# Kernel tuning notes

Hardware: AMD Instinct MI355X
Metric: run time of the kernel (lower is better)

Reference implementation:

```python
import jax, jax.numpy as jnp
import numpy as np

B, SQ, SK, D, H, DFF = 4, 1024, 1024, 1024, 16, 4096
DEPTH = D // H
EPS = 1e-6


def setup_inputs() -> dict:
    key = jax.random.key(0)
    ks = jax.random.split(key, 32)
    s = 0.02
    inp = {
        "x": jax.random.normal(ks[0], (B, SQ, D), jnp.float32),
        "enc_output": jax.random.normal(ks[1], (B, SK, D), jnp.float32),
        # causal look-ahead mask: 1 where attention is disallowed
        "look_ahead_mask": (1.0 - jnp.tril(jnp.ones((SQ, SQ), jnp.float32)))[None, None],
        "padding_mask": jnp.zeros((B, 1, 1, SK), jnp.float32),
    }
    names = ["wq1", "wk1", "wv1", "wo1", "wq2", "wk2", "wv2", "wo2"]
    for i, n in enumerate(names):
        inp[n] = jax.random.normal(ks[2 + i], (D, D), jnp.float32) * s
        inp["b" + n[1:]] = jnp.zeros((D,), jnp.float32)
    inp["w_ffn1"] = jax.random.normal(ks[12], (D, DFF), jnp.float32) * s
    inp["b_ffn1"] = jnp.zeros((DFF,), jnp.float32)
    inp["w_ffn2"] = jax.random.normal(ks[13], (DFF, D), jnp.float32) * s
    inp["b_ffn2"] = jnp.zeros((D,), jnp.float32)
    for i in (1, 2, 3):
        inp[f"gamma{i}"] = jnp.ones((D,), jnp.float32)
        inp[f"beta{i}"] = jnp.zeros((D,), jnp.float32)
    return inp


def _layernorm(x, gamma, beta):
    mu = jnp.mean(x, axis=-1, keepdims=True)
    var = jnp.var(x, axis=-1, keepdims=True)
    return (x - mu) * jax.lax.rsqrt(var + EPS) * gamma + beta


def _split_heads(x):
    b, s, _ = x.shape
    return x.reshape(b, s, H, DEPTH).transpose(0, 2, 1, 3)  # (B,H,S,depth)


def _mha(v_in, k_in, q_in, mask, wq, bq, wk, bk, wv, bv, wo, bo):
    q = _split_heads(q_in @ wq + bq)
    k = _split_heads(k_in @ wk + bk)
    v = _split_heads(v_in @ wv + bv)
    logits = jnp.einsum("bhqd,bhkd->bhqk", q, k) / jnp.sqrt(jnp.float32(DEPTH))
    if mask is not None:
        logits = logits + mask * -1e9
    attn = jax.nn.softmax(logits, axis=-1)
    out = jnp.einsum("bhqk,bhkd->bhqd", attn, v)
    out = out.transpose(0, 2, 1, 3).reshape(q_in.shape[0], -1, D)
    return out @ wo + bo, attn


def reference(x, enc_output, look_ahead_mask, padding_mask,
              wq1, bq1, wk1, bk1, wv1, bv1, wo1, bo1,
              wq2, bq2, wk2, bk2, wv2, bv2, wo2, bo2,
              w_ffn1, b_ffn1, w_ffn2, b_ffn2,
              gamma1, beta1, gamma2, beta2, gamma3, beta3):
    attn1, aw1 = _mha(x, x, x, look_ahead_mask,
                      wq1, bq1, wk1, bk1, wv1, bv1, wo1, bo1)
    out1 = _layernorm(attn1 + x, gamma1, beta1)
    attn2, aw2 = _mha(enc_output, enc_output, out1, padding_mask,
                      wq2, bq2, wk2, bk2, wv2, bv2, wo2, bo2)
    out2 = _layernorm(attn2 + out1, gamma2, beta2)
    ffn = jax.nn.relu(out2 @ w_ffn1 + b_ffn1) @ w_ffn2 + b_ffn2
    out3 = _layernorm(ffn + out2, gamma3, beta3)
    return out3, aw1, aw2
```

## Files before the change

### kernel.cpp

```cpp
#include <hip/hip_runtime.h>

#define NB 4
#define SEQ 1024
#define DM 1024
#define NH 16
#define DEP 64
#define DFFN 4096

typedef __attribute__((ext_vector_type(8))) short short8;
typedef __attribute__((ext_vector_type(4))) float f32x4;
typedef __attribute__((ext_vector_type(4))) unsigned short us4;

__device__ __forceinline__ unsigned short f2bf(float f) {
    union { float f; unsigned int u; } v; v.f = f;
    unsigned int u = v.u;
    return (unsigned short)((u + 0x7FFFu + ((u >> 16) & 1u)) >> 16);
}

__device__ __forceinline__ void gload16(const void* g, void* l) {
    __builtin_amdgcn_global_load_lds((const __attribute__((address_space(1))) unsigned int*)g,
                                     (__attribute__((address_space(3))) unsigned int*)l, 16, 0, 0);
}

__global__ __launch_bounds__(256) void cast2_kernel(const float* __restrict__ a,
                                                    const float* __restrict__ b,
                                                    unsigned short* __restrict__ oa,
                                                    unsigned short* __restrict__ ob, int n4) {
    int i = blockIdx.x * 256 + threadIdx.x;
    const float* in = blockIdx.y ? b : a;
    unsigned short* out = blockIdx.y ? ob : oa;
    if (i < n4) {
        f32x4 f = __builtin_nontemporal_load((const f32x4*)in + i);
        us4 u;
        u[0] = f2bf(f[0]); u[1] = f2bf(f[1]); u[2] = f2bf(f[2]); u[3] = f2bf(f[3]);
        ((us4*)out)[i] = u;
    }
}

struct P10 { const float* p[10]; };
__global__ __launch_bounds__(256) void castTall_kernel(P10 s,
                                                       unsigned short* __restrict__ wsq,
                                                       unsigned short* __restrict__ wf1t,
                                                       unsigned short* __restrict__ wf2t) {
    __shared__ float tile[64][65];
    const int tid = blockIdx.x, t = threadIdx.x;
    const float* in; unsigned short* out; int R, C, r0, c0;
    if (tid < 2048) {
        int wi = tid >> 8, t2 = tid & 255;
        in = s.p[wi]; out = wsq + (size_t)wi * DM * DM; R = DM; C = DM;
        r0 = (t2 >> 4) * 64; c0 = (t2 & 15) * 64;
    } else if (tid < 3072) {
        int t2 = tid - 2048;
        in = s.p[8]; out = wf1t; R = DM; C = DFFN;
        r0 = (t2 >> 6) * 64; c0 = (t2 & 63) * 64;
    } else {
        int t2 = tid - 3072;
        in = s.p[9]; out = wf2t; R = DFFN; C = DM;
        r0 = (t2 >> 4) * 64; c0 = (t2 & 15) * 64;
    }
#pragma unroll
    for (int p = 0; p < 4; ++p) {
        int r = p * 16 + (t >> 4), c = (t & 15) * 4;
        f32x4 f = __builtin_nontemporal_load((const f32x4*)(in + (size_t)(r0 + r) * C + c0 + c));
        tile[r][c] = f[0]; tile[r][c + 1] = f[1]; tile[r][c + 2] = f[2]; tile[r][c + 3] = f[3];
    }
    __syncthreads();
#pragma unroll
    for (int p = 0; p < 4; ++p) {
        int n = p * 16 + (t >> 4), k = (t & 15) * 4;
        us4 u;
#pragma unroll
        for (int j = 0; j < 4; ++j) u[j] = f2bf(tile[k + j][n]);
        *(us4*)(out + (size_t)(c0 + n) * R + r0 + k) = u;
    }
}

__global__ __launch_bounds__(256) void biaspack_kernel(const float* __restrict__ bq1,
                                                       const float* __restrict__ bk1,
                                                       const float* __restrict__ bv1,
                                                       const float* __restrict__ bk2,
                                                       const float* __restrict__ bv2,
                                                       float* __restrict__ bqkv1,
                                                       float* __restrict__ bkv2) {
    int i = blockIdx.x * 256 + threadIdx.x;
    if (i < 1024) bqkv1[i] = bq1[i];
    else if (i < 2048) bqkv1[i] = bk1[i - 1024];
    else if (i < 3072) bqkv1[i] = bv1[i - 2048];
    else if (i < 4096) bkv2[i - 3072] = bk2[i - 3072];
    else if (i < 5120) bkv2[i - 3072] = bv2[i - 4096];
}

template <int BM, int BN, int BK, int RELU, int WB, int WF, int WVT>
__global__ __launch_bounds__(256) void gemm_kernel(const unsigned short* __restrict__ A,
                                                   const unsigned short* __restrict__ Wt,
                                                   const float* __restrict__ bias,
                                                   unsigned short* __restrict__ Cb,
                                                   float* __restrict__ Cf,
                                                   unsigned short* __restrict__ Vt,
                                                   int vstart,
                                                   int M, int N, int K) {
    constexpr int AM = BM / 32;
    constexpr int BT = BN / 32;
    constexpr int KS = BK / 32;
    constexpr int LPR = BK / 8;
    constexpr int RPI = 64 / LPR;
    constexpr int AR = (BM / 4) / RPI;
    constexpr int BR = (BN / 4) / RPI;
    constexpr int NLD = AR + BR;
    __shared__ unsigned short As[3][BM * BK];
    __shared__ unsigned short Bs[3][BN * BK];
    const int t = threadIdx.x;
    const int lane = t & 63, w = t >> 6;
    const int nwg = gridDim.x * gridDim.y;
    const int rawid = blockIdx.y * gridDim.x + blockIdx.x;
    const int swz = (rawid & 7) * (nwg >> 3) + (rawid >> 3);
    const int m0 = (swz / gridDim.x) * BM, n0 = (swz % gridDim.x) * BN;
    const int wm = (w >> 1) * (BM / 2), wn = (w & 1) * (BN / 2);
    const int lr = lane & 15, g = lane >> 4, kb = g * 8;
    const int srow = lane / LPR;
    const int sslotl = lane % LPR;
    const int sswz = (BK == 64) ? (sslotl ^ srow) : sslotl;
    const int scol = sswz * 8;
    const int nk = K / BK;

    f32x4 acc[AM][BT];
#pragma unroll
    for (int a = 0; a < AM; ++a)
#pragma unroll
        for (int b = 0; b < BT; ++b)
#pragma unroll
            for (int j = 0; j < 4; ++j) acc[a][b][j] = 0.f;

    auto STAGE = [&](int buf, int kt) {
#pragma unroll
        for (int ia = 0; ia < AR; ++ia) {
            int rb = w * (BM / 4) + ia * RPI;
            gload16(A + (size_t)(m0 + rb + srow) * K + kt + scol, &As[buf][rb * BK]);
        }
#pragma unroll
        for (int ib = 0; ib < BR; ++ib) {
            int rb = w * (BN / 4) + ib * RPI;
            gload16(Wt + (size_t)(n0 + rb + srow) * K + kt + scol, &Bs[buf][rb * BK]);
        }
    };

    STAGE(0, 0);
    if (nk > 1) STAGE(1, BK);
    int sb = 2, cb = 0;
    for (int i = 0; i < nk; ++i) {
        if (i + 2 < nk) {
            STAGE(sb, (i + 2) * BK);
            if (++sb == 3) sb = 0;
            asm volatile("s_waitcnt vmcnt(%0)" :: "n"(2 * NLD) : "memory");
        } else if (i + 1 < nk) {
            asm volatile("s_waitcnt vmcnt(%0)" :: "n"(NLD) : "memory");
        } else {
            asm volatile("s_waitcnt vmcnt(0)" ::: "memory");
        }
        __builtin_amdgcn_s_barrier();

        short8 af[AM][KS], bfr[BT][KS];
#pragma unroll
        for (int ii = 0; ii < AM; ++ii)
#pragma unroll
            for (int ks = 0; ks < KS; ++ks) {
                int ofs = (BK == 64) ? (((ks * 4 + g) ^ (lr & 7)) << 3) : (ks * 32 + kb);
                af[ii][ks] = *(const short8*)&As[cb][(wm + ii * 16 + lr) * BK + ofs];
            }
#pragma unroll
        for (int ii = 0; ii < BT; ++ii)
#pragma unroll
            for (int ks = 0; ks < KS; ++ks) {
                int ofs = (BK == 64) ? (((ks * 4 + g) ^ (lr & 7)) << 3) : (ks * 32 + kb);
                bfr[ii][ks] = *(const short8*)&Bs[cb][(wn + ii * 16 + lr) * BK + ofs];
            }
#pragma unroll
        for (int ks = 0; ks < KS; ++ks)
#pragma unroll
            for (int am = 0; am < AM; ++am)
#pragma unroll
                for (int bn = 0; bn < BT; ++bn)
                    acc[am][bn] = __builtin_amdgcn_mfma_f32_16x16x32_bf16(af[am][ks], bfr[bn][ks], acc[am][bn], 0, 0, 0);
        if (++cb == 3) cb = 0;
        __builtin_amdgcn_s_barrier();
    }

#pragma unroll
    for (int am = 0; am < AM; ++am) {
#pragma unroll
        for (int bn = 0; bn < BT; ++bn) {
            int col = n0 + wn + bn * 16 + lr;
            float bv = bias ? bias[col] : 0.f;
            int rowb = m0 + wm + am * 16 + g * 4;
            float vv[4];
#pragma unroll
            for (int i = 0; i < 4; ++i) {
                float v = acc[am][bn][i] + bv;
                if (RELU) v = v > 0.f ? v : 0.f;
                vv[i] = v;
                if (WF) Cf[(size_t)(rowb + i) * N + col] = v;
                if (WB) Cb[(size_t)(rowb + i) * N + col] = f2bf(v);
            }
            if (WVT && col >= vstart) {
                int h = (col - vstart) >> 6, dep = (col - vstart) & 63;
                int b = rowb >> 10, kpos = rowb & 1023;
                us4 u;
#pragma unroll
                for (int i = 0; i < 4; ++i) u[i] = f2bf(vv[i]);
                *(us4*)(Vt + ((size_t)(b * NH + h) * DEP + dep) * SEQ + kpos) = u;
            }
        }
    }
}

template <int CAUSAL>
__global__ __launch_bounds__(256, 2) void attn_kernel(const unsigned short* __restrict__ Q, int ldq,
                                                      const unsigned short* __restrict__ Kp, int ldk,
                                                      const unsigned short* __restrict__ Vt,
                                                      const float* __restrict__ pad,
                                                      float* __restrict__ aw,
                                                      unsigned short* __restrict__ ctx) {
    __shared__ unsigned short Ks[3][128 * 64];
    __shared__ unsigned short Pch[32 * 128];
    __shared__ float redm[4][32];
    __shared__ float reds[4][32];
    const int t = threadIdx.x, lane = t & 63, w = t >> 6;
    const int lr = lane & 15, g = lane >> 4;
    const int id = blockIdx.x;
    const int bh = (id & 7) + ((id >> 8) << 3);
    const int qt = (id >> 3) & 31;
    const int q0 = qt * 32;
    const int b = bh >> 4, h = bh & 15;
    const size_t qbase = (size_t)b * SEQ * ldq + (size_t)h * DEP;
    const size_t kbase = (size_t)b * SEQ * ldk + (size_t)h * DEP;
    const int cmax = CAUSAL ? (q0 >> 7) + 1 : 8;

    const int srow = lane >> 3;
    const int sslot = (lane & 7) ^ srow;

    short8 aq[2][2];
#pragma unroll
    for (int p = 0; p < 2; ++p)
#pragma unroll
        for (int ks = 0; ks < 2; ++ks)
            aq[p][ks] = *(const short8*)(Q + qbase + (size_t)(q0 + p * 16 + lr) * ldq + ks * 32 + g * 8);

    f32x4 acc[2][8][2];
#pragma unroll
    for (int p = 0; p < 2; ++p)
#pragma unroll
        for (int c = 0; c < 8; ++c)
#pragma unroll
            for (int bn = 0; bn < 2; ++bn)
#pragma unroll
                for (int j = 0; j < 4; ++j) acc[p][c][bn][j] = 0.f;

#define STAGE_K(BUF, CH)                                                                   \
    {                                                                                      \
        _Pragma("unroll") for (int i_ = 0; i_ < 4; ++i_) {                                 \
            int rb_ = w * 32 + i_ * 8;                                                     \
            gload16(Kp + kbase + (size_t)((CH) * 128 + rb_ + srow) * ldk + sslot * 8,      \
                    &Ks[BUF][rb_ * 64]);                                                   \
        }                                                                                  \
    }

    STAGE_K(0, 0);
    if (1 < cmax) STAGE_K(1, 1);
#pragma unroll
    for (int c = 0; c < 8; ++c) {
        if (c < cmax) {
            if (c + 2 < cmax) {
                STAGE_K((c + 2) % 3, c + 2);
                asm volatile("s_waitcnt vmcnt(8)" ::: "memory");
            } else if (c + 1 < cmax) {
                asm volatile("s_waitcnt vmcnt(4)" ::: "memory");
            } else {
                asm volatile("s_waitcnt vmcnt(0)" ::: "memory");
            }
            __builtin_amdgcn_s_setprio(1);
#pragma unroll
            for (int ks = 0; ks < 2; ++ks)
#pragma unroll
                for (int bn = 0; bn < 2; ++bn) {
                    int row = w * 32 + bn * 16 + lr;
                    short8 bk = *(const short8*)((const char*)&Ks[c % 3][0] + row * 128 +
                                                 ((ks * 64 + g * 16) ^ ((lr & 7) << 4)));
                    acc[0][c][bn] = __builtin_amdgcn_mfma_f32_16x16x32_bf16(bk, aq[0][ks], acc[0][c][bn], 0, 0, 0);
                    acc[1][c][bn] = __builtin_amdgcn_mfma_f32_16x16x32_bf16(bk, aq[1][ks], acc[1][c][bn], 0, 0, 0);
                }
            __builtin_amdgcn_s_setprio(0);
        }
    }
#undef STAGE_K

    float mrow[2] = {-1e30f, -1e30f};
#pragma unroll
    for (int c = 0; c < 8; ++c) {
        if (c < cmax) {
#pragma unroll
            for (int bn = 0; bn < 2; ++bn) {
                int k4 = c * 128 + w * 32 + bn * 16 + g * 4;
                f32x4 pv = {0.f, 0.f, 0.f, 0.f};
                if (pad) pv = *(const f32x4*)(pad + (size_t)b * SEQ + k4);
#pragma unroll
                for (int p = 0; p < 2; ++p) {
                    int q = q0 + p * 16 + lr;
#pragma unroll
                    for (int i = 0; i < 4; ++i) {
                        float v = acc[p][c][bn][i] * 0.125f + pv[i] * -1e9f;
                        if (CAUSAL && (k4 + i) > q) v = -1e30f;
                        acc[p][c][bn][i] = v;
                        mrow[p] = fmaxf(mrow[p], v);
                    }
                }
            }
        }
    }
#pragma unroll
    for (int p = 0; p < 2; ++p) {
        mrow[p] = fmaxf(mrow[p], __shfl_xor(mrow[p], 16));
        mrow[p] = fmaxf(mrow[p], __shfl_xor(mrow[p], 32));
    }
    if (lane < 16) { redm[w][lr] = mrow[0]; redm[w][16 + lr] = mrow[1]; }
    __syncthreads();
    float Mv[2];
#pragma unroll
    for (int p = 0; p < 2; ++p)
        Mv[p] = fmaxf(fmaxf(redm[0][p * 16 + lr], redm[1][p * 16 + lr]),
                      fmaxf(redm[2][p * 16 + lr], redm[3][p * 16 + lr]));

    float srw[2] = {0.f, 0.f};
#pragma unroll
    for (int c = 0; c < 8; ++c) {
        if (c < cmax) {
#pragma unroll
            for (int p = 0; p < 2; ++p)
#pragma unroll
                for (int bn = 0; bn < 2; ++bn)
#pragma unroll
                    for (int i = 0; i < 4; ++i) {
                        float e = __expf(acc[p][c][bn][i] - Mv[p]);
                        acc[p][c][bn][i] = e;
                        srw[p] += e;
                    }
        }
    }
#pragma unroll
    for (int p = 0; p < 2; ++p) {
        srw[p] += __shfl_xor(srw[p], 16);
        srw[p] += __shfl_xor(srw[p], 32);
    }
    if (lane < 16) { reds[w][lr] = srw[0]; reds[w][16 + lr] = srw[1]; }
    __syncthreads();
    float inv[2];
#pragma unroll
    for (int p = 0; p < 2; ++p)
        inv[p] = 1.0f / (reds[0][p * 16 + lr] + reds[1][p * 16 + lr] +
                         reds[2][p * 16 + lr] + reds[3][p * 16 + lr]);

    f32x4 acc2[2];
#pragma unroll
    for (int p = 0; p < 2; ++p)
#pragma unroll
        for (int j = 0; j < 4; ++j) acc2[p][j] = 0.f;
    char* pch = (char*)Pch;
    const int sw = (lr & 7) << 4;
#pragma unroll
    for (int c = 0; c < 8; ++c) {
        if (c < cmax) {
            __syncthreads();
#pragma unroll
            for (int p = 0; p < 2; ++p)
#pragma unroll
                for (int bn = 0; bn < 2; ++bn) {
                    us4 u;
#pragma unroll
                    for (int i = 0; i < 4; ++i) u[i] = f2bf(acc[p][c][bn][i] * inv[p]);
                    *(us4*)(pch + (p * 16 + lr) * 256 + ((w * 64 + bn * 32 + g * 8) ^ sw)) = u;
                }
            __syncthreads();
            __builtin_amdgcn_s_setprio(1);
#pragma unroll
            for (int ks = 0; ks < 4; ++ks) {
                short8 bf = *(const short8*)(Vt + ((size_t)bh * DEP + w * 16 + lr) * SEQ + c * 128 + ks * 32 + g * 8);
#pragma unroll
                for (int p = 0; p < 2; ++p) {
                    short8 af = *(const short8*)(pch + (p * 16 + lr) * 256 + ((ks * 64 + g * 16) ^ sw));
                    acc2[p] = __builtin_amdgcn_mfma_f32_16x16x32_bf16(af, bf, acc2[p], 0, 0, 0);
                }
            }
            __builtin_amdgcn_s_setprio(0);
        }
    }
#pragma unroll
    for (int p = 0; p < 2; ++p)
#pragma unroll
        for (int i = 0; i < 4; ++i)
            ctx[((size_t)b * SEQ + q0 + p * 16 + g * 4 + i) * DM + h * DEP + w * 16 + lr] = f2bf(acc2[p][i]);

#pragma unroll
    for (int p = 0; p < 2; ++p) {
        float* awrow = aw + ((size_t)bh * SEQ + q0 + p * 16 + lr) * SEQ;
#pragma unroll
        for (int c = 0; c < 8; ++c)
#pragma unroll
            for (int bn = 0; bn < 2; ++bn) {
                f32x4 o = {0.f, 0.f, 0.f, 0.f};
                if (c < cmax) {
#pragma unroll
                    for (int i = 0; i < 4; ++i) o[i] = acc[p][c][bn][i] * inv[p];
                }
                __builtin_nontemporal_store(o, (f32x4*)(awrow + c * 128 + w * 32 + bn * 16 + g * 4));
            }
    }
}

template <int WB, int NTF>
__global__ __launch_bounds__(256) void ln_kernel(const float* __restrict__ X,
                                                 const float* __restrict__ R,
                                                 const float* __restrict__ gamma,
                                                 const float* __restrict__ beta,
                                                 float* __restrict__ outF,
                                                 unsigned short* __restrict__ outB) {
    size_t row = blockIdx.x;
    const int t = threadIdx.x;
    float4 a = ((const float4*)(X + (row << 10)))[t];
    float4 r = ((const float4*)(R + (row << 10)))[t];
    float v0 = a.x + r.x, v1 = a.y + r.y, v2 = a.z + r.z, v3 = a.w + r.w;
    float s = v0 + v1 + v2 + v3;
    float q = v0 * v0 + v1 * v1 + v2 * v2 + v3 * v3;
#pragma unroll
    for (int off = 32; off; off >>= 1) {
        s += __shfl_down(s, off);
        q += __shfl_down(q, off);
    }
    __shared__ float rs[4], rq[4];
    if ((t & 63) == 0) { rs[t >> 6] = s; rq[t >> 6] = q; }
    __syncthreads();
    s = rs[0] + rs[1] + rs[2] + rs[3];
    q = rq[0] + rq[1] + rq[2] + rq[3];
    float mean = s * (1.0f / 1024.0f);
    float var = q * (1.0f / 1024.0f) - mean * mean;
    float inv = rsqrtf(var + 1e-6f);
    float g0 = gamma[t * 4], g1 = gamma[t * 4 + 1], g2 = gamma[t * 4 + 2], g3 = gamma[t * 4 + 3];
    float b0 = beta[t * 4], b1 = beta[t * 4 + 1], b2 = beta[t * 4 + 2], b3 = beta[t * 4 + 3];
    f32x4 o;
    o[0] = (v0 - mean) * inv * g0 + b0;
    o[1] = (v1 - mean) * inv * g1 + b1;
    o[2] = (v2 - mean) * inv * g2 + b2;
    o[3] = (v3 - mean) * inv * g3 + b3;
    if (NTF) __builtin_nontemporal_store(o, (f32x4*)(outF + (row << 10)) + t);
    else ((f32x4*)(outF + (row << 10)))[t] = o;
    if (WB) {
        us4 u;
        u[0] = f2bf(o[0]); u[1] = f2bf(o[1]); u[2] = f2bf(o[2]); u[3] = f2bf(o[3]);
        ((us4*)(outB + (row << 10)))[t] = u;
    }
}

extern "C" void kernel_launch(void* const* d_in, const int* in_sizes, int n_in,
                              void* d_out, int out_size, void* d_ws, size_t ws_size,
                              hipStream_t stream) {
    const float* x = (const float*)d_in[0];
    const float* enc = (const float*)d_in[1];
    const float* pad = (const float*)d_in[3];
    const float* wq1 = (const float*)d_in[4];  const float* bq1 = (const float*)d_in[5];
    const float* wk1 = (const float*)d_in[6];  const float* bk1 = (const float*)d_in[7];
    const float* wv1 = (const float*)d_in[8];  const float* bv1 = (const float*)d_in[9];
    const float* wo1 = (const float*)d_in[10]; const float* bo1 = (const float*)d_in[11];
    const float* wq2 = (const float*)d_in[12]; const float* bq2 = (const float*)d_in[13];
    const float* wk2 = (const float*)d_in[14]; const float* bk2 = (const float*)d_in[15];
    const float* wv2 = (const float*)d_in[16]; const float* bv2 = (const float*)d_in[17];
    const float* wo2 = (const float*)d_in[18]; const float* bo2 = (const float*)d_in[19];
    const float* wf1 = (const float*)d_in[20]; const float* bf1 = (const float*)d_in[21];
    const float* wf2 = (const float*)d_in[22]; const float* bf2 = (const float*)d_in[23];
    const float* g1 = (const float*)d_in[24]; const float* be1 = (const float*)d_in[25];
    const float* g2 = (const float*)d_in[26]; const float* be2 = (const float*)d_in[27];
    const float* g3 = (const float*)d_in[28]; const float* be3 = (const float*)d_in[29];

    float* out3 = (float*)d_out;
    float* aw1 = out3 + (size_t)NB * SEQ * DM;
    float* aw2 = aw1 + (size_t)NB * NH * SEQ * SEQ;

    char* ws = (char*)d_ws;
    size_t off = 0;
    auto take = [&](size_t n) { char* p = ws + off; off += (n + 255) & ~(size_t)255; return p; };
    const size_t SZ_SD_BF = (size_t)NB * SEQ * DM * 2;
    const size_t SZ_SD_F  = (size_t)NB * SEQ * DM * 4;
    const size_t SZ_DD_BF = (size_t)DM * DM * 2;

    unsigned short* wqkv1t = (unsigned short*)take(3 * SZ_DD_BF);
    unsigned short* wq2t   = (unsigned short*)take(SZ_DD_BF);
    unsigned short* wkv2t  = (unsigned short*)take(2 * SZ_DD_BF);
    unsigned short* wo1t   = (unsigned short*)take(SZ_DD_BF);
    unsigned short* wo2t   = (unsigned short*)take(SZ_DD_BF);
    unsigned short* wf1t   = (unsigned short*)take((size_t)DM * DFFN * 2);
    unsigned short* wf2t   = (unsigned short*)take((size_t)DFFN * DM * 2);
    float* bqkv1 = (float*)take(3 * DM * 4);
    float* bkv2  = (float*)take(2 * DM * 4);
    unsigned short* xb    = (unsigned short*)take(SZ_SD_BF);
    unsigned short* encb  = (unsigned short*)take(SZ_SD_BF);
    unsigned short* qkv1b = (unsigned short*)take(3 * SZ_SD_BF);
    unsigned short* v1t   = (unsigned short*)take(SZ_SD_BF);
    unsigned short* qb    = (unsigned short*)take(SZ_SD_BF);
    unsigned short* kv2b  = (unsigned short*)take(2 * SZ_SD_BF);
    unsigned short* v2t   = (unsigned short*)take(SZ_SD_BF);
    unsigned short* ctx   = (unsigned short*)take(SZ_SD_BF);
    float* goutf  = (float*)take(SZ_SD_F);
    float* out1f  = (float*)take(SZ_SD_F);
    unsigned short* out1b = (unsigned short*)take(SZ_SD_BF);
    float* out2f  = (float*)take(SZ_SD_F);
    unsigned short* out2b = (unsigned short*)take(SZ_SD_BF);
    unsigned short* ffn1b = (unsigned short*)take((size_t)NB * SEQ * DFFN * 2);

    {
        int n4 = NB * SEQ * DM / 4;
        dim3 gc((n4 + 255) / 256, 2);
        cast2_kernel<<<gc, 256, 0, stream>>>(x, enc, xb, encb, n4);
    }
    {
        P10 s;
        s.p[0] = wq1; s.p[1] = wk1; s.p[2] = wv1; s.p[3] = wq2;
        s.p[4] = wk2; s.p[5] = wv2; s.p[6] = wo1; s.p[7] = wo2;
        s.p[8] = wf1; s.p[9] = wf2;
        castTall_kernel<<<4096, 256, 0, stream>>>(s, wqkv1t, wf1t, wf2t);
    }
    biaspack_kernel<<<20, 256, 0, stream>>>(bq1, bk1, bv1, bk2, bv2, bqkv1, bkv2);

    const int M = NB * SEQ;
    dim3 gQKV(3 * DM / 256, M / 128);
    dim3 gKV(2 * DM / 256, M / 128);
    dim3 gDD64(DM / 128, M / 64);
    dim3 gDF(DFFN / 256, M / 128);

    gemm_kernel<128, 256, 32, 0, 1, 0, 1><<<gQKV, 256, 0, stream>>>(xb, wqkv1t, bqkv1, qkv1b, nullptr, v1t, 2048, M, 3 * DM, DM);
    attn_kernel<1><<<2048, 256, 0, stream>>>(qkv1b, 3 * DM, qkv1b + DM, 3 * DM, v1t, nullptr, aw1, ctx);
    gemm_kernel<64, 128, 64, 0, 0, 1, 0><<<gDD64, 256, 0, stream>>>(ctx, wo1t, bo1, nullptr, goutf, nullptr, 0, M, DM, DM);
    ln_kernel<1, 0><<<M, 256, 0, stream>>>(goutf, x, g1, be1, out1f, out1b);

    gemm_kernel<64, 128, 64, 0, 1, 0, 0><<<gDD64, 256, 0, stream>>>(out1b, wq2t, bq2, qb, nullptr, nullptr, 0, M, DM, DM);
    gemm_kernel<128, 256, 32, 0, 1, 0, 1><<<gKV, 256, 0, stream>>>(encb, wkv2t, bkv2, kv2b, nullptr, v2t, 1024, M, 2 * DM, DM);
    attn_kernel<0><<<2048, 256, 0, stream>>>(qb, DM, kv2b, 2 * DM, v2t, pad, aw2, ctx);
    gemm_kernel<64, 128, 64, 0, 0, 1, 0><<<gDD64, 256, 0, stream>>>(ctx, wo2t, bo2, nullptr, goutf, nullptr, 0, M, DM, DM);
    ln_kernel<1, 0><<<M, 256, 0, stream>>>(goutf, out1f, g2, be2, out2f, out2b);

    gemm_kernel<128, 256, 32, 1, 1, 0, 0><<<gDF, 256, 0, stream>>>(out2b, wf1t, bf1, ffn1b, nullptr, nullptr, 0, M, DFFN, DM);
    gemm_kernel<64, 128, 64, 0, 0, 1, 0><<<gDD64, 256, 0, stream>>>(ffn1b, wf2t, bf2, nullptr, goutf, nullptr, 0, M, DM, DFFN);
    ln_kernel<0, 1><<<M, 256, 0, stream>>>(goutf, out2f, g3, be3, out3, nullptr);
}
```

Measured before the change: 561.8 us.

## Fuse self-attn QKV and cross-attn KV projections into one GEMM, shrink tiles

Merges the QKV projection on x and the KV projection on the encoder output into a single 5*DM-wide GEMM launch. Blocks pick their A operand by column range, and each writes to the matching output and V-transpose buffers. Weights and biases are packed contiguously in the new order to support this. GEMM tiles for the fused and FFN1 GEMMs shrink from 128x256 to 128x128, with BT fixed at 4, and s_setprio is raised around the MFMA block; the aim is more blocks in flight and one fewer launch, at the cost of less data reuse per tile.

```diff
diff --git a/kernel.cpp b/kernel.cpp
--- a/kernel.cpp
+++ b/kernel.cpp
@@ -80,27 +80,27 @@
                                                        const float* __restrict__ bv1,
                                                        const float* __restrict__ bk2,
                                                        const float* __restrict__ bv2,
-                                                       float* __restrict__ bqkv1,
-                                                       float* __restrict__ bkv2) {
+                                                       float* __restrict__ bf) {
     int i = blockIdx.x * 256 + threadIdx.x;
-    if (i < 1024) bqkv1[i] = bq1[i];
-    else if (i < 2048) bqkv1[i] = bk1[i - 1024];
-    else if (i < 3072) bqkv1[i] = bv1[i - 2048];
-    else if (i < 4096) bkv2[i - 3072] = bk2[i - 3072];
-    else if (i < 5120) bkv2[i - 3072] = bv2[i - 4096];
-}
-
-template <int BM, int BN, int BK, int RELU, int WB, int WF, int WVT>
+    if (i < 1024) bf[i] = bq1[i];
+    else if (i < 2048) bf[i] = bk1[i - 1024];
+    else if (i < 3072) bf[i] = bv1[i - 2048];
+    else if (i < 4096) bf[i] = bk2[i - 3072];
+    else if (i < 5120) bf[i] = bv2[i - 4096];
+}
+
+template <int BM, int BN, int BK, int RELU, int WB, int WF, int FUSED>
 __global__ __launch_bounds__(256) void gemm_kernel(const unsigned short* __restrict__ A,
+                                                   const unsigned short* __restrict__ A2,
                                                    const unsigned short* __restrict__ Wt,
                                                    const float* __restrict__ bias,
                                                    unsigned short* __restrict__ Cb,
+                                                   unsigned short* __restrict__ Cb2,
                                                    float* __restrict__ Cf,
-                                                   unsigned short* __restrict__ Vt,
-                                                   int vstart,
+                                                   unsigned short* __restrict__ Vt1,
+                                                   unsigned short* __restrict__ Vt2,
                                                    int M, int N, int K) {
     constexpr int AM = BM / 32;
-    constexpr int BT = BN / 32;
     constexpr int KS = BK / 32;
     constexpr int LPR = BK / 8;
     constexpr int RPI = 64 / LPR;
@@ -122,12 +122,13 @@
     const int sswz = (BK == 64) ? (sslotl ^ srow) : sslotl;
     const int scol = sswz * 8;
     const int nk = K / BK;
-
-    f32x4 acc[AM][BT];
+    const unsigned short* Ause = (FUSED && n0 >= 3072) ? A2 : A;
+
+    f32x4 acc[AM][4];
 #pragma unroll
     for (int a = 0; a < AM; ++a)
 #pragma unroll
-        for (int b = 0; b < BT; ++b)
+        for (int b = 0; b < 4; ++b)
 #pragma unroll
             for (int j = 0; j < 4; ++j) acc[a][b][j] = 0.f;
 
@@ -135,7 +136,7 @@
 #pragma unroll
         for (int ia = 0; ia < AR; ++ia) {
             int rb = w * (BM / 4) + ia * RPI;
-            gload16(A + (size_t)(m0 + rb + srow) * K + kt + scol, &As[buf][rb * BK]);
+            gload16(Ause + (size_t)(m0 + rb + srow) * K + kt + scol, &As[buf][rb * BK]);
         }
 #pragma unroll
         for (int ib = 0; ib < BR; ++ib) {
@@ -159,7 +160,7 @@
         }
         __builtin_amdgcn_s_barrier();
 
-        short8 af[AM][KS], bfr[BT][KS];
+        short8 af[AM][KS], bfr[4][KS];
 #pragma unroll
         for (int ii = 0; ii < AM; ++ii)
 #pragma unroll
@@ -168,19 +169,21 @@
                 af[ii][ks] = *(const short8*)&As[cb][(wm + ii * 16 + lr) * BK + ofs];
             }
 #pragma unroll
-        for (int ii = 0; ii < BT; ++ii)
+        for (int ii = 0; ii < 4; ++ii)
 #pragma unroll
             for (int ks = 0; ks < KS; ++ks) {
                 int ofs = (BK == 64) ? (((ks * 4 + g) ^ (lr & 7)) << 3) : (ks * 32 + kb);
                 bfr[ii][ks] = *(const short8*)&Bs[cb][(wn + ii * 16 + lr) * BK + ofs];
             }
+        __builtin_amdgcn_s_setprio(1);
 #pragma unroll
         for (int ks = 0; ks < KS; ++ks)
 #pragma unroll
             for (int am = 0; am < AM; ++am)
 #pragma unroll
-                for (int bn = 0; bn < BT; ++bn)
+                for (int bn = 0; bn < 4; ++bn)
                     acc[am][bn] = __builtin_amdgcn_mfma_f32_16x16x32_bf16(af[am][ks], bfr[bn][ks], acc[am][bn], 0, 0, 0);
+        __builtin_amdgcn_s_setprio(0);
         if (++cb == 3) cb = 0;
         __builtin_amdgcn_s_barrier();
     }
@@ -188,26 +191,44 @@
 #pragma unroll
     for (int am = 0; am < AM; ++am) {
 #pragma unroll
-        for (int bn = 0; bn < BT; ++bn) {
+        for (int bn = 0; bn < 4; ++bn) {
             int col = n0 + wn + bn * 16 + lr;
             float bv = bias ? bias[col] : 0.f;
             int rowb = m0 + wm + am * 16 + g * 4;
             float vv[4];
+            us4 ub;
 #pragma unroll
             for (int i = 0; i < 4; ++i) {
                 float v = acc[am][bn][i] + bv;
                 if (RELU) v = v > 0.f ? v : 0.f;
                 vv[i] = v;
-                if (WF) Cf[(size_t)(rowb + i) * N + col] = v;
-                if (WB) Cb[(size_t)(rowb + i) * N + col] = f2bf(v);
-            }
-            if (WVT && col >= vstart) {
-                int h = (col - vstart) >> 6, dep = (col - vstart) & 63;
-                int b = rowb >> 10, kpos = rowb & 1023;
-                us4 u;
-#pragma unroll
-                for (int i = 0; i < 4; ++i) u[i] = f2bf(vv[i]);
-                *(us4*)(Vt + ((size_t)(b * NH + h) * DEP + dep) * SEQ + kpos) = u;
+                ub[i] = f2bf(v);
+            }
+            if (!FUSED) {
+#pragma unroll
+                for (int i = 0; i < 4; ++i) {
+                    if (WF) Cf[(size_t)(rowb + i) * N + col] = vv[i];
+                    if (WB) Cb[(size_t)(rowb + i) * N + col] = ub[i];
+                }
+            } else {
+                if (col < 3072) {
+#pragma unroll
+                    for (int i = 0; i < 4; ++i) Cb[(size_t)(rowb + i) * 3072 + col] = ub[i];
+                    if (col >= 2048) {
+                        int h = (col - 2048) >> 6, dep = (col - 2048) & 63;
+                        int b = rowb >> 10, kpos = rowb & 1023;
+                        *(us4*)(Vt1 + ((size_t)(b * NH + h) * DEP + dep) * SEQ + kpos) = ub;
+                    }
+                } else {
+                    int c2 = col - 3072;
+#pragma unroll
+                    for (int i = 0; i < 4; ++i) Cb2[(size_t)(rowb + i) * 2048 + c2] = ub[i];
+                    if (col >= 4096) {
+                        int h = (col - 4096) >> 6, dep = (col - 4096) & 63;
+                        int b = rowb >> 10, kpos = rowb & 1023;
+                        *(us4*)(Vt2 + ((size_t)(b * NH + h) * DEP + dep) * SEQ + kpos) = ub;
+                    }
+                }
             }
         }
     }
@@ -489,15 +510,14 @@
     const size_t SZ_SD_F  = (size_t)NB * SEQ * DM * 4;
     const size_t SZ_DD_BF = (size_t)DM * DM * 2;
 
-    unsigned short* wqkv1t = (unsigned short*)take(3 * SZ_DD_BF);
-    unsigned short* wq2t   = (unsigned short*)take(SZ_DD_BF);
-    unsigned short* wkv2t  = (unsigned short*)take(2 * SZ_DD_BF);
-    unsigned short* wo1t   = (unsigned short*)take(SZ_DD_BF);
-    unsigned short* wo2t   = (unsigned short*)take(SZ_DD_BF);
-    unsigned short* wf1t   = (unsigned short*)take((size_t)DM * DFFN * 2);
-    unsigned short* wf2t   = (unsigned short*)take((size_t)DFFN * DM * 2);
-    float* bqkv1 = (float*)take(3 * DM * 4);
-    float* bkv2  = (float*)take(2 * DM * 4);
+    unsigned short* wsq   = (unsigned short*)take(8 * SZ_DD_BF);
+    unsigned short* wfus  = wsq;
+    unsigned short* wq2t  = wsq + 5ul * DM * DM;
+    unsigned short* wo1t  = wsq + 6ul * DM * DM;
+    unsigned short* wo2t  = wsq + 7ul * DM * DM;
+    unsigned short* wf1t  = (unsigned short*)take((size_t)DM * DFFN * 2);
+    unsigned short* wf2t  = (unsigned short*)take((size_t)DFFN * DM * 2);
+    float* bfus = (float*)take(5 * DM * 4);
     unsigned short* xb    = (unsigned short*)take(SZ_SD_BF);
     unsigned short* encb  = (unsigned short*)take(SZ_SD_BF);
     unsigned short* qkv1b = (unsigned short*)take(3 * SZ_SD_BF);
@@ -520,31 +540,36 @@
     }
     {
         P10 s;
-        s.p[0] = wq1; s.p[1] = wk1; s.p[2] = wv1; s.p[3] = wq2;
-        s.p[4] = wk2; s.p[5] = wv2; s.p[6] = wo1; s.p[7] = wo2;
+        s.p[0] = wq1; s.p[1] = wk1; s.p[2] = wv1; s.p[3] = wk2;
+        s.p[4] = wv2; s.p[5] = wq2; s.p[6] = wo1; s.p[7] = wo2;
         s.p[8] = wf1; s.p[9] = wf2;
-        castTall_kernel<<<4096, 256, 0, stream>>>(s, wqkv1t, wf1t, wf2t);
-    }
-    biaspack_kernel<<<20, 256, 0, stream>>>(bq1, bk1, bv1, bk2, bv2, bqkv1, bkv2);
+        castTall_kernel<<<4096, 256, 0, stream>>>(s, wsq, wf1t, wf2t);
+    }
+    biaspack_kernel<<<20, 256, 0, stream>>>(bq1, bk1, bv1, bk2, bv2, bfus);
 
     const int M = NB * SEQ;
-    dim3 gQKV(3 * DM / 256, M / 128);
-    dim3 gKV(2 * DM / 256, M / 128);
+    dim3 gFUS(5 * DM / 128, M / 128);
     dim3 gDD64(DM / 128, M / 64);
-    dim3 gDF(DFFN / 256, M / 128);
-
-    gemm_kernel<128, 256, 32, 0, 1, 0, 1><<<gQKV, 256, 0, stream>>>(xb, wqkv1t, bqkv1, qkv1b, nullptr, v1t, 2048, M, 3 * DM, DM);
+    dim3 gDF(DFFN / 128, M / 128);
+
+    gemm_kernel<128, 128, 32, 0, 1, 0, 1><<<gFUS, 256, 0, stream>>>(
+        xb, encb, wfus, bfus, qkv1b, kv2b, nullptr, v1t, v2t, M, 5 * DM, DM);
+
     attn_kernel<1><<<2048, 256, 0, stream>>>(qkv1b, 3 * DM, qkv1b + DM, 3 * DM, v1t, nullptr, aw1, ctx);
-    gemm_kernel<64, 128, 64, 0, 0, 1, 0><<<gDD64, 256, 0, stream>>>(ctx, wo1t, bo1, nullptr, goutf, nullptr, 0, M, DM, DM);
+    gemm_kernel<64, 128, 64, 0, 0, 1, 0><<<gDD64, 256, 0, stream>>>(
+        ctx, nullptr, wo1t, bo1, nullptr, nullptr, goutf, nullptr, nullptr, M, DM, DM);
     ln_kernel<1, 0><<<M, 256, 0, stream>>>(goutf, x, g1, be1, out1f, out1b);
 
-    gemm_kernel<64, 128, 64, 0, 1, 0, 0><<<gDD64, 256, 0, stream>>>(out1b, wq2t, bq2, qb, nullptr, nullptr, 0, M, DM, DM);
-    gemm_kernel<128, 256, 32, 0, 1, 0, 1><<<gKV, 256, 0, stream>>>(encb, wkv2t, bkv2, kv2b, nullptr, v2t, 1024, M, 2 * DM, DM);
+    gemm_kernel<64, 128, 64, 0, 1, 0, 0><<<gDD64, 256, 0, stream>>>(
+        out1b, nullptr, wq2t, bq2, qb, nullptr, nullptr, nullptr, nullptr, M, DM, DM);
     attn_kernel<0><<<2048, 256, 0, stream>>>(qb, DM, kv2b, 2 * DM, v2t, pad, aw2, ctx);
-    gemm_kernel<64, 128, 64, 0, 0, 1, 0><<<gDD64, 256, 0, stream>>>(ctx, wo2t, bo2, nullptr, goutf, nullptr, 0, M, DM, DM);
+    gemm_kernel<64, 128, 64, 0, 0, 1, 0><<<gDD64, 256, 0, stream>>>(
+        ctx, nullptr, wo2t, bo2, nullptr, nullptr, goutf, nullptr, nullptr, M, DM, DM);
     ln_kernel<1, 0><<<M, 256, 0, stream>>>(goutf, out1f, g2, be2, out2f, out2b);
 
-    gemm_kernel<128, 256, 32, 1, 1, 0, 0><<<gDF, 256, 0, stream>>>(out2b, wf1t, bf1, ffn1b, nullptr, nullptr, 0, M, DFFN, DM);
-    gemm_kernel<64, 128, 64, 0, 0, 1, 0><<<gDD64, 256, 0, stream>>>(ffn1b, wf2t, bf2, nullptr, goutf, nullptr, 0, M, DM, DFFN);
+    gemm_kernel<128, 128, 32, 1, 1, 0, 0><<<gDF, 256, 0, stream>>>(
+        out2b, nullptr, wf1t, bf1, ffn1b, nullptr, nullptr, nullptr, nullptr, M, DFFN, DM);
+    gemm_kernel<64, 128, 64, 0, 0, 1, 0><<<gDD64, 256, 0, stream>>>(
+        ffn1b, nullptr, wf2t, bf2, nullptr, nullptr, goutf, nullptr, nullptr, M, DM, DFFN);
     ln_kernel<0, 1><<<M, 256, 0, stream>>>(goutf, out2f, g3, be3, out3, nullptr);
 }
```

Result: faster. 500.5 us (-10.9%).
